# Performance work log

Hardware: AMD Instinct MI355X
Metric: run time of the kernel (lower is better)

The kernel has to match this reference:

```python
import jax, jax.numpy as jnp
import numpy as np

D_MODEL = 1024
NUM_HEADS = 16
D_K = D_MODEL // NUM_HEADS


def setup_inputs() -> dict:
    key = jax.random.key(0)
    ks = jax.random.split(key, 5)
    B, S = 4, 2048
    scale = 1.0 / np.sqrt(D_MODEL)
    x = jax.random.normal(ks[0], (B, S, D_MODEL), dtype=jnp.float32)
    Wq = jax.random.normal(ks[1], (D_MODEL, D_MODEL), dtype=jnp.float32) * scale
    Wk = jax.random.normal(ks[2], (D_MODEL, D_MODEL), dtype=jnp.float32) * scale
    Wv = jax.random.normal(ks[3], (D_MODEL, D_MODEL), dtype=jnp.float32) * scale
    Wo = jax.random.normal(ks[4], (D_MODEL, D_MODEL), dtype=jnp.float32) * scale
    return {"x": x, "Wq": Wq, "Wk": Wk, "Wv": Wv, "Wo": Wo}


def reference(x, Wq, Wk, Wv, Wo):
    B, S, _ = x.shape
    # projections (torch Linear: y = x @ W^T, no bias)
    def proj(W):
        y = jnp.einsum('bsd,ed->bse', x, W)
        # split heads: (b, s, h*dk) -> (b, h, s, dk)
        return y.reshape(B, S, NUM_HEADS, D_K).transpose(0, 2, 1, 3)
    Q, K, V = proj(Wq), proj(Wk), proj(Wv)
    scores = jnp.einsum('bhqd,bhkd->bhqk', Q, K) / np.sqrt(D_K)
    causal = jnp.tril(jnp.ones((S, S), dtype=bool))
    scores = jnp.where(causal, scores, -jnp.inf)
    attn = jax.nn.softmax(scores, axis=-1)
    out = jnp.einsum('bhqk,bhkd->bhqd', attn, V)
    out = out.transpose(0, 2, 1, 3).reshape(B, S, D_MODEL)
    return jnp.einsum('bse,de->bsd', out, Wo)
```

## Files before the change

### kernel.cpp

```cpp
#include <hip/hip_runtime.h>
#include <hip/hip_bf16.h>

typedef __attribute__((ext_vector_type(8))) short short8;
typedef __attribute__((ext_vector_type(4))) float f32x4;

static constexpr int DM = 1024;
static constexpr int NH = 16;
static constexpr int DK = 64;
static constexpr int SL = 2048;
static constexpr int BB = 4;
static constexpr size_t QKV_ELEMS = (size_t)BB * NH * SL * DK;
static constexpr float NEG_BIG = -30000.0f;
static constexpr float SC_LOG2E = 0.125f * 1.44269504088896340736f;

union PackB { __hip_bfloat16 h[8]; uint4 u; };
union Pack4 { __hip_bfloat16 h[4]; uint2 u; };

typedef __attribute__((address_space(1))) unsigned int gu32;
typedef __attribute__((address_space(3))) unsigned int lu32;
__device__ __forceinline__ void async_copy16(const void* g, void* l) {
    __builtin_amdgcn_global_load_lds((gu32*)g, (lu32*)l, 16, 0, 0);
}

__global__ __launch_bounds__(256)
void cvt_all(const float* __restrict__ x,
             const float* __restrict__ wq, const float* __restrict__ wk,
             const float* __restrict__ wv, const float* __restrict__ wo,
             __hip_bfloat16* __restrict__ dst)
{
    const size_t i = (size_t)blockIdx.x * 256 + threadIdx.x;
    const float* src; size_t local;
    if (i < 2097152) { src = x; local = i; }
    else {
        const size_t j = i - 2097152;
        const int r = (int)(j >> 18);
        local = j & 262143;
        src = (r == 0) ? wq : (r == 1) ? wk : (r == 2) ? wv : wo;
    }
    float4 f = reinterpret_cast<const float4*>(src)[local];
    Pack4 p;
    p.h[0] = __float2bfloat16(f.x); p.h[1] = __float2bfloat16(f.y);
    p.h[2] = __float2bfloat16(f.z); p.h[3] = __float2bfloat16(f.w);
    reinterpret_cast<uint2*>(dst)[i] = p.u;
}

template<int MODE>
__global__ __launch_bounds__(256)
void gemm_lds(const __hip_bfloat16* __restrict__ A,
              const __hip_bfloat16* __restrict__ W,
              void* __restrict__ outp)
{
    __shared__ __hip_bfloat16 As[128 * 32];
    __shared__ __hip_bfloat16 Bs[128 * 32];
    const int tid  = threadIdx.x;
    const int m0   = blockIdx.x * 128;
    const int n0   = blockIdx.y * 128;
    const int w    = tid >> 6;
    const int lane = tid & 63;
    const int quad = lane >> 4;
    const int ln   = lane & 15;
    const int wm   = (w & 1) * 64;
    const int wn   = (w >> 1) * 64;

    const int srow   = lane >> 2;
    const int schunk = (lane & 3) * 8;

    f32x4 acc[4][4] = {};

    for (int k0 = 0; k0 < DM; k0 += 32) {
        #pragma unroll
        for (int j = 0; j < 2; j++) {
            const int rbase = w * 32 + j * 16;
            async_copy16(A + (size_t)(m0 + rbase + srow) * DM + k0 + schunk,
                         &As[rbase * 32]);
            async_copy16(W + (size_t)(n0 + rbase + srow) * DM + k0 + schunk,
                         &Bs[rbase * 32]);
        }
        __syncthreads();

        short8 a[4], b[4];
        #pragma unroll
        for (int i = 0; i < 4; i++)
            a[i] = *reinterpret_cast<const short8*>(&As[(wm + i*16 + ln) * 32 + quad*8]);
        #pragma unroll
        for (int j = 0; j < 4; j++)
            b[j] = *reinterpret_cast<const short8*>(&Bs[(wn + j*16 + ln) * 32 + quad*8]);
        #pragma unroll
        for (int i = 0; i < 4; i++)
            #pragma unroll
            for (int j = 0; j < 4; j++)
                acc[i][j] = __builtin_amdgcn_mfma_f32_16x16x32_bf16(a[i], b[j], acc[i][j], 0, 0, 0);
        __syncthreads();
    }

    #pragma unroll
    for (int i = 0; i < 4; i++) {
        #pragma unroll
        for (int j = 0; j < 4; j++) {
            #pragma unroll
            for (int r = 0; r < 4; r++) {
                const int m = m0 + wm + i*16 + quad*4 + r;
                const int n = n0 + wn + j*16 + ln;
                const float v = acc[i][j][r];
                if (MODE == 2) {
                    ((float*)outp)[(size_t)m * DM + n] = v;
                } else {
                    const int b_ = m >> 11;
                    const int s  = m & 2047;
                    const int h  = n >> 6;
                    const int d  = n & 63;
                    size_t idx;
                    if (MODE == 0) idx = ((size_t)((b_*NH + h)*SL + s))*DK + d;
                    else           idx = ((size_t)((b_*NH + h)*DK + d))*SL + s;
                    ((__hip_bfloat16*)outp)[idx] = __float2bfloat16(v);
                }
            }
        }
    }
}

template<bool A_BF16, int MODE>
__global__ __launch_bounds__(256)
void gemm_bt(const void* __restrict__ Ap,
             const float* __restrict__ W,
             void* __restrict__ outp)
{
    __shared__ __hip_bfloat16 As[128][40];
    __shared__ __hip_bfloat16 Bs[128][40];
    const int tid  = threadIdx.x;
    const int m0   = blockIdx.x * 128;
    const int n0   = blockIdx.y * 128;
    const int w    = tid >> 6;
    const int lane = tid & 63;
    const int quad = lane >> 4;
    const int ln   = lane & 15;
    const int wm   = (w & 1) * 64;
    const int wn   = (w >> 1) * 64;
    const int lr   = tid >> 1;
    const int lc   = (tid & 1) * 16;

    f32x4 acc[4][4] = {};

    for (int k0 = 0; k0 < DM; k0 += 32) {
        if (A_BF16) {
            const uint4* ap = reinterpret_cast<const uint4*>(
                (const __hip_bfloat16*)Ap + (size_t)(m0 + lr) * DM + k0 + lc);
            uint4 a0 = ap[0], a1 = ap[1];
            *reinterpret_cast<uint4*>(&As[lr][lc])     = a0;
            *reinterpret_cast<uint4*>(&As[lr][lc + 8]) = a1;
        } else {
            const float4* ap = reinterpret_cast<const float4*>(
                (const float*)Ap + (size_t)(m0 + lr) * DM + k0 + lc);
            float4 f0 = ap[0], f1 = ap[1], f2 = ap[2], f3 = ap[3];
            PackB p0, p1;
            p0.h[0] = __float2bfloat16(f0.x); p0.h[1] = __float2bfloat16(f0.y);
            p0.h[2] = __float2bfloat16(f0.z); p0.h[3] = __float2bfloat16(f0.w);
            p0.h[4] = __float2bfloat16(f1.x); p0.h[5] = __float2bfloat16(f1.y);
            p0.h[6] = __float2bfloat16(f1.z); p0.h[7] = __float2bfloat16(f1.w);
            p1.h[0] = __float2bfloat16(f2.x); p1.h[1] = __float2bfloat16(f2.y);
            p1.h[2] = __float2bfloat16(f2.z); p1.h[3] = __float2bfloat16(f2.w);
            p1.h[4] = __float2bfloat16(f3.x); p1.h[5] = __float2bfloat16(f3.y);
            p1.h[6] = __float2bfloat16(f3.z); p1.h[7] = __float2bfloat16(f3.w);
            *reinterpret_cast<uint4*>(&As[lr][lc])     = p0.u;
            *reinterpret_cast<uint4*>(&As[lr][lc + 8]) = p1.u;
        }
        {
            const float4* wp = reinterpret_cast<const float4*>(
                W + (size_t)(n0 + lr) * DM + k0 + lc);
            float4 f0 = wp[0], f1 = wp[1], f2 = wp[2], f3 = wp[3];
            PackB p0, p1;
            p0.h[0] = __float2bfloat16(f0.x); p0.h[1] = __float2bfloat16(f0.y);
            p0.h[2] = __float2bfloat16(f0.z); p0.h[3] = __float2bfloat16(f0.w);
            p0.h[4] = __float2bfloat16(f1.x); p0.h[5] = __float2bfloat16(f1.y);
            p0.h[6] = __float2bfloat16(f1.z); p0.h[7] = __float2bfloat16(f1.w);
            p1.h[0] = __float2bfloat16(f2.x); p1.h[1] = __float2bfloat16(f2.y);
            p1.h[2] = __float2bfloat16(f2.z); p1.h[3] = __float2bfloat16(f2.w);
            p1.h[4] = __float2bfloat16(f3.x); p1.h[5] = __float2bfloat16(f3.y);
            p1.h[6] = __float2bfloat16(f3.z); p1.h[7] = __float2bfloat16(f3.w);
            *reinterpret_cast<uint4*>(&Bs[lr][lc])     = p0.u;
            *reinterpret_cast<uint4*>(&Bs[lr][lc + 8]) = p1.u;
        }
        __syncthreads();

        short8 a[4], b[4];
        #pragma unroll
        for (int i = 0; i < 4; i++)
            a[i] = *reinterpret_cast<const short8*>(&As[wm + i*16 + ln][quad*8]);
        #pragma unroll
        for (int j = 0; j < 4; j++)
            b[j] = *reinterpret_cast<const short8*>(&Bs[wn + j*16 + ln][quad*8]);
        #pragma unroll
        for (int i = 0; i < 4; i++)
            #pragma unroll
            for (int j = 0; j < 4; j++)
                acc[i][j] = __builtin_amdgcn_mfma_f32_16x16x32_bf16(a[i], b[j], acc[i][j], 0, 0, 0);
        __syncthreads();
    }

    #pragma unroll
    for (int i = 0; i < 4; i++) {
        #pragma unroll
        for (int j = 0; j < 4; j++) {
            #pragma unroll
            for (int r = 0; r < 4; r++) {
                const int m = m0 + wm + i*16 + quad*4 + r;
                const int n = n0 + wn + j*16 + ln;
                const float v = acc[i][j][r];
                if (MODE == 2) {
                    ((float*)outp)[(size_t)m * DM + n] = v;
                } else {
                    const int b_ = m >> 11;
                    const int s  = m & 2047;
                    const int h  = n >> 6;
                    const int d  = n & 63;
                    size_t idx;
                    if (MODE == 0) idx = ((size_t)((b_*NH + h)*SL + s))*DK + d;
                    else           idx = ((size_t)((b_*NH + h)*DK + d))*SL + s;
                    ((__hip_bfloat16*)outp)[idx] = __float2bfloat16(v);
                }
            }
        }
    }
}

__global__ __launch_bounds__(256)
void attn_causal(const __hip_bfloat16* __restrict__ Q,
                 const __hip_bfloat16* __restrict__ K,
                 const __hip_bfloat16* __restrict__ Vt,
                 __hip_bfloat16* __restrict__ O)
{
    __shared__ __hip_bfloat16 Ks[64][72];
    __shared__ __hip_bfloat16 Vs[64][72];
    __shared__ __hip_bfloat16 p_lds[4][16][72];

    const int tid  = threadIdx.x;
    const int w    = tid >> 6;
    const int lane = tid & 63;
    const int quad = lane >> 4;
    const int ln   = lane & 15;
    const int bh   = blockIdx.y;
    const int b_   = bh >> 4;
    const int h    = bh & 15;

    const int srow   = tid >> 3;
    const int schunk = (tid & 7) * 8;

    const __hip_bfloat16* Qb = Q  + (size_t)bh * SL * DK;
    const __hip_bfloat16* Kb = K  + (size_t)bh * SL * DK;
    const __hip_bfloat16* Vb = Vt + (size_t)bh * DK * SL;

    for (int pass = 0; pass < 2; ++pass) {
        const int qt    = (pass == 0) ? (int)blockIdx.x : 31 - (int)blockIdx.x;
        const int q0    = qt * 64;
        const int qbase = q0 + w * 16;

        short8 aq0 = *reinterpret_cast<const short8*>(Qb + (size_t)(qbase + ln) * DK + quad*8);
        short8 aq1 = *reinterpret_cast<const short8*>(Qb + (size_t)(qbase + ln) * DK + 32 + quad*8);

        f32x4 acc[4] = {};
        float lsum[4] = {0.f, 0.f, 0.f, 0.f};

        for (int k0 = 0; k0 <= q0; k0 += 64) {
            const __hip_bfloat16* Kg = Kb + (size_t)(k0 + srow) * DK + schunk;
            uint4 kv0 = *reinterpret_cast<const uint4*>(Kg);
            uint4 kv1 = *reinterpret_cast<const uint4*>(Kg + 32 * DK);
            const __hip_bfloat16* Vg = Vb + (size_t)srow * SL + k0 + schunk;
            uint4 vv0 = *reinterpret_cast<const uint4*>(Vg);
            uint4 vv1 = *reinterpret_cast<const uint4*>(Vg + 32 * SL);
            __syncthreads();
            *reinterpret_cast<uint4*>(&Ks[srow     ][schunk]) = kv0;
            *reinterpret_cast<uint4*>(&Ks[srow + 32][schunk]) = kv1;
            *reinterpret_cast<uint4*>(&Vs[srow     ][schunk]) = vv0;
            *reinterpret_cast<uint4*>(&Vs[srow + 32][schunk]) = vv1;
            __syncthreads();

            f32x4 s[4];
            #pragma unroll
            for (int kc = 0; kc < 4; kc++) {
                short8 bk0 = *reinterpret_cast<const short8*>(&Ks[kc*16 + ln][quad*8]);
                short8 bk1 = *reinterpret_cast<const short8*>(&Ks[kc*16 + ln][32 + quad*8]);
                f32x4 z = {};
                z = __builtin_amdgcn_mfma_f32_16x16x32_bf16(aq0, bk0, z, 0, 0, 0);
                z = __builtin_amdgcn_mfma_f32_16x16x32_bf16(aq1, bk1, z, 0, 0, 0);
                s[kc] = z;
            }
            const bool diag = (k0 == q0);
            #pragma unroll
            for (int kc = 0; kc < 4; kc++) {
                #pragma unroll
                for (int r = 0; r < 4; r++) {
                    float v = s[kc][r] * SC_LOG2E;
                    if (diag) {
                        const int kg = k0 + kc*16 + ln;
                        const int qg = qbase + quad*4 + r;
                        if (kg > qg) v = NEG_BIG;
                    }
                    const float p = __builtin_amdgcn_exp2f(v);
                    lsum[r] += p;
                    p_lds[w][quad*4 + r][kc*16 + ln] = __float2bfloat16(p);
                }
            }
            short8 ap0 = *reinterpret_cast<const short8*>(&p_lds[w][ln][quad*8]);
            short8 ap1 = *reinterpret_cast<const short8*>(&p_lds[w][ln][32 + quad*8]);
            #pragma unroll
            for (int nt = 0; nt < 4; nt++) {
                short8 bv0 = *reinterpret_cast<const short8*>(&Vs[nt*16 + ln][quad*8]);
                short8 bv1 = *reinterpret_cast<const short8*>(&Vs[nt*16 + ln][32 + quad*8]);
                acc[nt] = __builtin_amdgcn_mfma_f32_16x16x32_bf16(ap0, bv0, acc[nt], 0, 0, 0);
                acc[nt] = __builtin_amdgcn_mfma_f32_16x16x32_bf16(ap1, bv1, acc[nt], 0, 0, 0);
            }
        }

        #pragma unroll
        for (int r = 0; r < 4; r++) {
            float v = lsum[r];
            v += __shfl_xor(v, 1, 64);
            v += __shfl_xor(v, 2, 64);
            v += __shfl_xor(v, 4, 64);
            v += __shfl_xor(v, 8, 64);
            lsum[r] = v;
        }

        #pragma unroll
        for (int nt = 0; nt < 4; nt++) {
            #pragma unroll
            for (int r = 0; r < 4; r++) {
                const int sI = qbase + quad*4 + r;
                const int d  = nt*16 + ln;
                const float v = acc[nt][r] / lsum[r];
                O[(((size_t)b_ * SL + sI) * NH + h) * DK + d] = __float2bfloat16(v);
            }
        }
    }
}

extern "C" void kernel_launch(void* const* d_in, const int* in_sizes, int n_in,
                              void* d_out, int out_size, void* d_ws, size_t ws_size,
                              hipStream_t stream)
{
    const float* x  = (const float*)d_in[0];
    const float* Wq = (const float*)d_in[1];
    const float* Wk = (const float*)d_in[2];
    const float* Wv = (const float*)d_in[3];
    const float* Wo = (const float*)d_in[4];

    __hip_bfloat16* q_ws = (__hip_bfloat16*)d_ws;
    __hip_bfloat16* k_ws = q_ws + QKV_ELEMS;
    __hip_bfloat16* v_ws = k_ws + QKV_ELEMS;
    __hip_bfloat16* obuf = (__hip_bfloat16*)d_out;
    float*          fbuf = (float*)d_ws;

    const dim3 gg(64, 8), gb(256);
    const size_t FAST_WS = (3 * QKV_ELEMS + QKV_ELEMS + 4 * (size_t)DM * DM)
                           * sizeof(__hip_bfloat16);

    if (ws_size >= FAST_WS) {
        __hip_bfloat16* xb  = v_ws + QKV_ELEMS;
        __hip_bfloat16* wqb = xb  + QKV_ELEMS;
        __hip_bfloat16* wkb = wqb + (size_t)DM * DM;
        __hip_bfloat16* wvb = wkb + (size_t)DM * DM;
        __hip_bfloat16* wob = wvb + (size_t)DM * DM;

        cvt_all<<<12288, 256, 0, stream>>>(x, Wq, Wk, Wv, Wo, xb);

        gemm_lds<0><<<gg, gb, 0, stream>>>(xb, wqb, q_ws);
        gemm_lds<0><<<gg, gb, 0, stream>>>(xb, wkb, k_ws);
        gemm_lds<1><<<gg, gb, 0, stream>>>(xb, wvb, v_ws);

        attn_causal<<<dim3(16, BB*NH), 256, 0, stream>>>(q_ws, k_ws, v_ws, obuf);

        gemm_lds<2><<<gg, gb, 0, stream>>>(obuf, wob, fbuf);
    } else {
        gemm_bt<false, 0><<<gg, gb, 0, stream>>>(x, Wq, q_ws);
        gemm_bt<false, 0><<<gg, gb, 0, stream>>>(x, Wk, k_ws);
        gemm_bt<false, 1><<<gg, gb, 0, stream>>>(x, Wv, v_ws);

        attn_causal<<<dim3(16, BB*NH), 256, 0, stream>>>(q_ws, k_ws, v_ws, obuf);

        gemm_bt<true, 2><<<gg, gb, 0, stream>>>(obuf, Wo, fbuf);
    }

    (void)hipMemcpyAsync(d_out, fbuf, QKV_ELEMS * sizeof(float),
                         hipMemcpyDeviceToDevice, stream);
}
```

Measured before the change: 291.3 us.

## Fuse QKV projections into one GEMM and write output projection directly

Merges the three Q/K/V projection launches into a single GEMM over the concatenated weight matrix, routing each output tile to Q, K or V layout in the epilogue. The output projection now writes fp32 results straight into the output buffer, and the attention output reuses the bf16 input scratch. This removes the final device-to-device copy of the full output and two kernel launches. It adds a per-element branch in the QKV epilogue.

```diff
diff --git a/kernel.cpp b/kernel.cpp
--- a/kernel.cpp
+++ b/kernel.cpp
@@ -44,11 +44,12 @@
     reinterpret_cast<uint2*>(dst)[i] = p.u;
 }
 
-template<int MODE>
 __global__ __launch_bounds__(256)
-void gemm_lds(const __hip_bfloat16* __restrict__ A,
+void gemm_qkv(const __hip_bfloat16* __restrict__ A,
               const __hip_bfloat16* __restrict__ W,
-              void* __restrict__ outp)
+              __hip_bfloat16* __restrict__ q_out,
+              __hip_bfloat16* __restrict__ k_out,
+              __hip_bfloat16* __restrict__ v_out)
 {
     __shared__ __hip_bfloat16 As[128 * 32];
     __shared__ __hip_bfloat16 Bs[128 * 32];
@@ -61,7 +62,6 @@
     const int ln   = lane & 15;
     const int wm   = (w & 1) * 64;
     const int wn   = (w >> 1) * 64;
-
     const int srow   = lane >> 2;
     const int schunk = (lane & 3) * 8;
 
@@ -101,22 +101,81 @@
             for (int r = 0; r < 4; r++) {
                 const int m = m0 + wm + i*16 + quad*4 + r;
                 const int n = n0 + wn + j*16 + ln;
-                const float v = acc[i][j][r];
-                if (MODE == 2) {
-                    ((float*)outp)[(size_t)m * DM + n] = v;
-                } else {
-                    const int b_ = m >> 11;
-                    const int s  = m & 2047;
-                    const int h  = n >> 6;
-                    const int d  = n & 63;
-                    size_t idx;
-                    if (MODE == 0) idx = ((size_t)((b_*NH + h)*SL + s))*DK + d;
-                    else           idx = ((size_t)((b_*NH + h)*DK + d))*SL + s;
-                    ((__hip_bfloat16*)outp)[idx] = __float2bfloat16(v);
-                }
-            }
-        }
-    }
+                const int b_ = m >> 11;
+                const int s  = m & 2047;
+                const int which = n >> 10;
+                const int nn = n & 1023;
+                const int h  = nn >> 6;
+                const int d  = nn & 63;
+                const __hip_bfloat16 v = __float2bfloat16(acc[i][j][r]);
+                if (which == 0)
+                    q_out[((size_t)((b_*NH + h)*SL + s))*DK + d] = v;
+                else if (which == 1)
+                    k_out[((size_t)((b_*NH + h)*SL + s))*DK + d] = v;
+                else
+                    v_out[((size_t)((b_*NH + h)*DK + d))*SL + s] = v;
+            }
+        }
+    }
+}
+
+__global__ __launch_bounds__(256)
+void gemm_wo(const __hip_bfloat16* __restrict__ A,
+             const __hip_bfloat16* __restrict__ W,
+             float* __restrict__ outp)
+{
+    __shared__ __hip_bfloat16 As[128 * 32];
+    __shared__ __hip_bfloat16 Bs[128 * 32];
+    const int tid  = threadIdx.x;
+    const int m0   = blockIdx.x * 128;
+    const int n0   = blockIdx.y * 128;
+    const int w    = tid >> 6;
+    const int lane = tid & 63;
+    const int quad = lane >> 4;
+    const int ln   = lane & 15;
+    const int wm   = (w & 1) * 64;
+    const int wn   = (w >> 1) * 64;
+    const int srow   = lane >> 2;
+    const int schunk = (lane & 3) * 8;
+
+    f32x4 acc[4][4] = {};
+
+    for (int k0 = 0; k0 < DM; k0 += 32) {
+        #pragma unroll
+        for (int j = 0; j < 2; j++) {
+            const int rbase = w * 32 + j * 16;
+            async_copy16(A + (size_t)(m0 + rbase + srow) * DM + k0 + schunk,
+                         &As[rbase * 32]);
+            async_copy16(W + (size_t)(n0 + rbase + srow) * DM + k0 + schunk,
+                         &Bs[rbase * 32]);
+        }
+        __syncthreads();
+
+        short8 a[4], b[4];
+        #pragma unroll
+        for (int i = 0; i < 4; i++)
+            a[i] = *reinterpret_cast<const short8*>(&As[(wm + i*16 + ln) * 32 + quad*8]);
+        #pragma unroll
+        for (int j = 0; j < 4; j++)
+            b[j] = *reinterpret_cast<const short8*>(&Bs[(wn + j*16 + ln) * 32 + quad*8]);
+        #pragma unroll
+        for (int i = 0; i < 4; i++)
+            #pragma unroll
+            for (int j = 0; j < 4; j++)
+                acc[i][j] = __builtin_amdgcn_mfma_f32_16x16x32_bf16(a[i], b[j], acc[i][j], 0, 0, 0);
+        __syncthreads();
+    }
+
+    #pragma unroll
+    for (int i = 0; i < 4; i++)
+        #pragma unroll
+        for (int j = 0; j < 4; j++)
+            #pragma unroll
+            for (int r = 0; r < 4; r++) {
+                const int m = m0 + wm + i*16 + quad*4 + r;
+                const int n = n0 + wn + j*16 + ln;
+                outp[(size_t)m * DM + n] = acc[i][j][r];
+            }
 }
 
 template<bool A_BF16, int MODE>
@@ -347,39 +406,33 @@
     __hip_bfloat16* q_ws = (__hip_bfloat16*)d_ws;
     __hip_bfloat16* k_ws = q_ws + QKV_ELEMS;
     __hip_bfloat16* v_ws = k_ws + QKV_ELEMS;
-    __hip_bfloat16* obuf = (__hip_bfloat16*)d_out;
-    float*          fbuf = (float*)d_ws;
-
-    const dim3 gg(64, 8), gb(256);
+
+    const dim3 gb(256);
     const size_t FAST_WS = (3 * QKV_ELEMS + QKV_ELEMS + 4 * (size_t)DM * DM)
                            * sizeof(__hip_bfloat16);
 
     if (ws_size >= FAST_WS) {
         __hip_bfloat16* xb  = v_ws + QKV_ELEMS;
         __hip_bfloat16* wqb = xb  + QKV_ELEMS;
-        __hip_bfloat16* wkb = wqb + (size_t)DM * DM;
-        __hip_bfloat16* wvb = wkb + (size_t)DM * DM;
-        __hip_bfloat16* wob = wvb + (size_t)DM * DM;
+        __hip_bfloat16* wob = wqb + 3 * (size_t)DM * DM;
 
         cvt_all<<<12288, 256, 0, stream>>>(x, Wq, Wk, Wv, Wo, xb);
 
-        gemm_lds<0><<<gg, gb, 0, stream>>>(xb, wqb, q_ws);
-        gemm_lds<0><<<gg, gb, 0, stream>>>(xb, wkb, k_ws);
-        gemm_lds<1><<<gg, gb, 0, stream>>>(xb, wvb, v_ws);
-
-        attn_causal<<<dim3(16, BB*NH), 256, 0, stream>>>(q_ws, k_ws, v_ws, obuf);
-
-        gemm_lds<2><<<gg, gb, 0, stream>>>(obuf, wob, fbuf);
+        gemm_qkv<<<dim3(64, 24), gb, 0, stream>>>(xb, wqb, q_ws, k_ws, v_ws);
+
+        attn_causal<<<dim3(16, BB*NH), 256, 0, stream>>>(q_ws, k_ws, v_ws, xb);
+
+        gemm_wo<<<dim3(64, 8), gb, 0, stream>>>(xb, wob, (float*)d_out);
     } else {
+        __hip_bfloat16* obuf = (__hip_bfloat16*)d_out;
+        float*          fbuf = (float*)d_ws;
+        const dim3 gg(64, 8);
         gemm_bt<false, 0><<<gg, gb, 0, stream>>>(x, Wq, q_ws);
         gemm_bt<false, 0><<<gg, gb, 0, stream>>>(x, Wk, k_ws);
         gemm_bt<false, 1><<<gg, gb, 0, stream>>>(x, Wv, v_ws);
-
         attn_causal<<<dim3(16, BB*NH), 256, 0, stream>>>(q_ws, k_ws, v_ws, obuf);
-
         gemm_bt<true, 2><<<gg, gb, 0, stream>>>(obuf, Wo, fbuf);
-    }
-
-    (void)hipMemcpyAsync(d_out, fbuf, QKV_ELEMS * sizeof(float),
-                         hipMemcpyDeviceToDevice, stream);
-}
+        (void)hipMemcpyAsync(d_out, fbuf, QKV_ELEMS * sizeof(float),
+                             hipMemcpyDeviceToDevice, stream);
+    }
+}
```

New measurement: 284.6 us. -2.3%, faster.
